# Performance work log

Hardware: AMD Instinct MI355X
Metric: run time of the kernel (lower is better)

The kernel has to match this reference:

```python
import jax, jax.numpy as jnp
import numpy as np

B, D, T = 8192, 1024, 3          # batch, input_dim, num_tasks
E, HM, OM = 8, 2048, 512         # mmoe: experts, hidden, output
P, S, HC, OC = 3, 4, 1024, 256   # ple: specific, shared, hidden, output
TH, OUT = 256, 1                 # tower hidden, out_dim per task
EPS = 1e-5


def _ln(h):
    mu = jnp.mean(h, axis=-1, keepdims=True)
    v = jnp.mean((h - mu) ** 2, axis=-1, keepdims=True)
    return (h - mu) * jax.lax.rsqrt(v + EPS)


def setup_inputs() -> dict:
    key = jax.random.key(0)
    ks = iter(jax.random.split(key, 64))
    def w(*shape):
        return 0.02 * jax.random.normal(next(ks), shape, jnp.float32)
    z = lambda *s: jnp.zeros(s, jnp.float32)
    o = lambda *s: jnp.ones(s, jnp.float32)
    return {
        "x": jax.random.normal(next(ks), (B, D), jnp.float32),
        "mmoe_w1": w(E, D, HM), "mmoe_b1": z(E, HM), "mmoe_g": o(E, HM), "mmoe_be": z(E, HM),
        "mmoe_w2": w(E, HM, OM), "mmoe_b2": z(E, OM),
        "mmoe_gw": w(T, D, E), "mmoe_gb": z(T, E),
        "c0_sw1": w(S, OM, HC), "c0_sb1": z(S, HC), "c0_sg": o(S, HC), "c0_sbe": z(S, HC),
        "c0_sw2": w(S, HC, OC), "c0_sb2": z(S, OC),
        "c0_tw1": w(T, P, OM, HC), "c0_tb1": z(T, P, HC), "c0_tg": o(T, P, HC), "c0_tbe": z(T, P, HC),
        "c0_tw2": w(T, P, HC, OC), "c0_tb2": z(T, P, OC),
        "c0_gw": w(T, OM, P + S), "c0_gb": z(T, P + S),
        "c0_sgw": w(OM, T * P + S), "c0_sgb": z(T * P + S),
        "c1_sw1": w(S, OC, HC), "c1_sb1": z(S, HC), "c1_sg": o(S, HC), "c1_sbe": z(S, HC),
        "c1_sw2": w(S, HC, OC), "c1_sb2": z(S, OC),
        "c1_tw1": w(T, P, OC, HC), "c1_tb1": z(T, P, HC), "c1_tg": o(T, P, HC), "c1_tbe": z(T, P, HC),
        "c1_tw2": w(T, P, HC, OC), "c1_tb2": z(T, P, OC),
        "c1_gw": w(T, OC, P + S), "c1_gb": z(T, P + S),
        "tow_w1": w(T, OC, TH), "tow_b1": z(T, TH), "tow_w2": w(T, TH, OUT), "tow_b2": z(T, OUT),
    }


def _cgc(shared_in, task_in, sw1, sb1, sg, sbe, sw2, sb2,
         tw1, tb1, tg, tbe, tw2, tb2, gw, gb, sgw=None, sgb=None):
    # shared experts: [S, B, O]
    hs = jnp.einsum('bd,sdh->sbh', shared_in, sw1) + sb1[:, None, :]
    hs = jax.nn.relu(_ln(hs) * sg[:, None, :] + sbe[:, None, :])
    so = jnp.einsum('sbh,sho->sbo', hs, sw2) + sb2[:, None, :]
    # task-specific experts: [T, P, B, O]
    ht = jnp.einsum('tbd,tpdh->tpbh', task_in, tw1) + tb1[:, :, None, :]
    ht = jax.nn.relu(_ln(ht) * tg[:, :, None, :] + tbe[:, :, None, :])
    to = jnp.einsum('tpbh,tpho->tpbo', ht, tw2) + tb2[:, :, None, :]
    Tn, Pn, Bn, On = to.shape
    Sn = so.shape[0]
    # per-task expert bank: task-specific first, then shared (matches torch.cat order)
    ex = jnp.concatenate([to, jnp.broadcast_to(so[None], (Tn, Sn, Bn, On))], axis=1)
    gate = jax.nn.softmax(jnp.einsum('tbd,tde->tbe', task_in, gw) + gb[:, None, :], axis=-1)
    task_out = jnp.einsum('tbe,tebo->tbo', gate, ex)
    if sgw is None:
        return None, task_out
    all_ex = jnp.concatenate([to.reshape(Tn * Pn, Bn, On), so], axis=0)
    sgate = jax.nn.softmax(shared_in @ sgw + sgb, axis=-1)
    shared_out = jnp.einsum('be,ebo->bo', sgate, all_ex)
    return shared_out, task_out


def _fwd(x, mmoe_w1, mmoe_b1, mmoe_g, mmoe_be, mmoe_w2, mmoe_b2, mmoe_gw, mmoe_gb,
         c0_sw1, c0_sb1, c0_sg, c0_sbe, c0_sw2, c0_sb2,
         c0_tw1, c0_tb1, c0_tg, c0_tbe, c0_tw2, c0_tb2, c0_gw, c0_gb, c0_sgw, c0_sgb,
         c1_sw1, c1_sb1, c1_sg, c1_sbe, c1_sw2, c1_sb2,
         c1_tw1, c1_tb1, c1_tg, c1_tbe, c1_tw2, c1_tb2, c1_gw, c1_gb,
         tow_w1, tow_b1, tow_w2, tow_b2):
    # --- MMoE layer (dropout = identity in eval) ---
    h = jnp.einsum('bd,edh->ebh', x, mmoe_w1) + mmoe_b1[:, None, :]
    h = jax.nn.relu(_ln(h) * mmoe_g[:, None, :] + mmoe_be[:, None, :])
    eo = jnp.einsum('ebh,eho->ebo', h, mmoe_w2) + mmoe_b2[:, None, :]  # [E,B,OM]
    gate = jax.nn.softmax(jnp.einsum('bd,tde->tbe', x, mmoe_gw) + mmoe_gb[:, None, :], axis=-1)
    task_hs = jnp.einsum('tbe,ebo->tbo', gate, eo)  # [T,B,OM]
    shared_h = jnp.mean(task_hs, axis=0)            # 'mean' aggregate
    # --- PLE CGC layers ---
    shared_h, task_hs = _cgc(shared_h, task_hs, c0_sw1, c0_sb1, c0_sg, c0_sbe, c0_sw2, c0_sb2,
                             c0_tw1, c0_tb1, c0_tg, c0_tbe, c0_tw2, c0_tb2, c0_gw, c0_gb, c0_sgw, c0_sgb)
    _, task_hs = _cgc(shared_h, task_hs, c1_sw1, c1_sb1, c1_sg, c1_sbe, c1_sw2, c1_sb2,
                      c1_tw1, c1_tb1, c1_tg, c1_tbe, c1_tw2, c1_tb2, c1_gw, c1_gb)
    # --- task towers ---
    th = jax.nn.relu(jnp.einsum('tbo,toh->tbh', task_hs, tow_w1) + tow_b1[:, None, :])
    return jnp.einsum('tbh,tho->tbo', th, tow_w2) + tow_b2[:, None, :]  # [T,B,OUT]


def reference(x, mmoe_w1, mmoe_b1, mmoe_g, mmoe_be, mmoe_w2, mmoe_b2, mmoe_gw, mmoe_gb,
              c0_sw1, c0_sb1, c0_sg, c0_sbe, c0_sw2, c0_sb2,
              c0_tw1, c0_tb1, c0_tg, c0_tbe, c0_tw2, c0_tb2, c0_gw, c0_gb, c0_sgw, c0_sgb,
              c1_sw1, c1_sb1, c1_sg, c1_sbe, c1_sw2, c1_sb2,
              c1_tw1, c1_tb1, c1_tg, c1_tbe, c1_tw2, c1_tb2, c1_gw, c1_gb,
              tow_w1, tow_b1, tow_w2, tow_b2):
    return _fwd(x, mmoe_w1, mmoe_b1, mmoe_g, mmoe_be, mmoe_w2, mmoe_b2, mmoe_gw, mmoe_gb,
                c0_sw1, c0_sb1, c0_sg, c0_sbe, c0_sw2, c0_sb2,
                c0_tw1, c0_tb1, c0_tg, c0_tbe, c0_tw2, c0_tb2, c0_gw, c0_gb, c0_sgw, c0_sgb,
                c1_sw1, c1_sb1, c1_sg, c1_sbe, c1_sw2, c1_sb2,
                c1_tw1, c1_tb1, c1_tg, c1_tbe, c1_tw2, c1_tb2, c1_gw, c1_gb,
                tow_w1, tow_b1, tow_w2, tow_b2)
```

## Files before the change

kernel.cpp:

```cpp
#include <hip/hip_runtime.h>

typedef unsigned short u16;
typedef unsigned int   u32;
typedef __bf16  bf16x8 __attribute__((ext_vector_type(8)));
typedef float   f32x4  __attribute__((ext_vector_type(4)));

#define B_ 8192
#define DI __device__ __forceinline__

DI u16 f2bf(float f) {
  u32 u = __float_as_uint(f);
  u = (u + 0x7fffu + ((u >> 16) & 1u)) >> 16;
  return (u16)u;
}
DI float bf2f(u16 h) { return __uint_as_float(((u32)h) << 16); }

DI void gll(const u16* g, u16* l) {
  __builtin_amdgcn_global_load_lds(
      (const __attribute__((address_space(1))) void*)g,
      (__attribute__((address_space(3))) void*)l, 16, 0, 0);
}

__global__ __launch_bounds__(256) void transpose_cast(
    const float* __restrict__ W, u16* __restrict__ Wt, int K, int N) {
  __shared__ float tile[64][65];
  int g = blockIdx.z;
  int k0 = blockIdx.x * 64, n0 = blockIdx.y * 64;
  const float* Wg = W + (size_t)g * K * N;
  u16* Og = Wt + (size_t)g * N * K;
  int tid = threadIdx.x;
  int rr = tid >> 4, cc = (tid & 15) * 4;
#pragma unroll
  for (int r = 0; r < 4; ++r) {
    int k = rr + r * 16;
    float4 v = *(const float4*)(Wg + (size_t)(k0 + k) * N + n0 + cc);
    tile[k][cc] = v.x; tile[k][cc + 1] = v.y; tile[k][cc + 2] = v.z; tile[k][cc + 3] = v.w;
  }
  __syncthreads();
  int nr = tid >> 3, kc = (tid & 7) * 8;
#pragma unroll
  for (int p = 0; p < 2; ++p) {
    int n = nr + p * 32;
    u16 tmp[8];
#pragma unroll
    for (int j = 0; j < 8; ++j) tmp[j] = f2bf(tile[kc + j][n]);
    *(uint4*)(Og + (size_t)(n0 + n) * K + k0 + kc) = *(uint4*)tmp;
  }
}

__global__ __launch_bounds__(256) void cast_bf16k(const float* __restrict__ X, u16* __restrict__ Y) {
  size_t i = ((size_t)blockIdx.x * 256 + threadIdx.x) * 4;
  float4 v = *(const float4*)(X + i);
  u16 t[4] = { f2bf(v.x), f2bf(v.y), f2bf(v.z), f2bf(v.w) };
  *(uint2*)(Y + i) = *(uint2*)t;
}

#define BM 128
#define BK 32
#define LDK 32

template<int BN_>
__global__ __launch_bounds__(256) void gemm_t(
    const u16* __restrict__ A, long a_stride, int a_div, int a_g0,
    const u16* __restrict__ Wt, const float* __restrict__ bias,
    u16* __restrict__ C, long c_stride, int N, int K, int relu_flag) {
  constexpr int JT = BN_ / 32;
  constexpr int BROWS = BN_ / 4;
  int gz = blockIdx.z;
  const u16* Ag = A + (size_t)((a_g0 + gz) / a_div) * a_stride;
  const u16* Wg = Wt + (size_t)gz * N * K;
  u16* Cg = C + (size_t)gz * c_stride;
  int m0 = blockIdx.x * BM, n0 = blockIdx.y * BN_;

  __shared__ __align__(16) u16 As[BM * LDK];
  __shared__ __align__(16) u16 Bs[BN_ * LDK];

  int tid = threadIdx.x;
  int wv = tid >> 6, ln = tid & 63;
  int wm = (wv >> 1) * 64, wn = (wv & 1) * (BN_ / 2);
  int lr = ln & 15, lk = (ln >> 4) * 8;

  int sr = ln >> 2;
  int sc = (ln & 3) * 8;
  const u16* aG = Ag + (size_t)(m0 + wv * 32 + sr) * K + sc;
  const u16* bG = Wg + (size_t)(n0 + wv * BROWS + sr) * K + sc;
  u16* aL0 = As + (wv * 32) * LDK;
  u16* aL1 = aL0 + 16 * LDK;
  u16* bL0 = Bs + (wv * BROWS) * LDK;

  f32x4 acc[4][JT];
#pragma unroll
  for (int i = 0; i < 4; ++i)
#pragma unroll
    for (int j = 0; j < JT; ++j)
      acc[i][j] = (f32x4){0.f, 0.f, 0.f, 0.f};

  int nk = K / BK;
  for (int ks = 0; ks < nk; ++ks) {
    __syncthreads();
    gll(aG + ks * BK, aL0);
    gll(aG + ks * BK + (size_t)16 * K, aL1);
    gll(bG + ks * BK, bL0);
    if (BN_ == 128) gll(bG + ks * BK + (size_t)16 * K, bL0 + 16 * LDK);
    __syncthreads();
    bf16x8 af[4], bfr[JT];
#pragma unroll
    for (int i = 0; i < 4; ++i) {
      union { uint4 u; bf16x8 v; } ua;
      ua.u = *(const uint4*)(As + (wm + i * 16 + lr) * LDK + lk);
      af[i] = ua.v;
    }
#pragma unroll
    for (int j = 0; j < JT; ++j) {
      union { uint4 u; bf16x8 v; } ub;
      ub.u = *(const uint4*)(Bs + (wn + j * 16 + lr) * LDK + lk);
      bfr[j] = ub.v;
    }
#pragma unroll
    for (int i = 0; i < 4; ++i)
#pragma unroll
      for (int j = 0; j < JT; ++j)
        acc[i][j] = __builtin_amdgcn_mfma_f32_16x16x32_bf16(af[i], bfr[j], acc[i][j], 0, 0, 0);
  }

  int mr = (ln >> 4) * 4;
#pragma unroll
  for (int i = 0; i < 4; ++i) {
#pragma unroll
    for (int j = 0; j < JT; ++j) {
      int n = n0 + wn + j * 16 + lr;
      float bv = bias[(size_t)gz * N + n];
#pragma unroll
      for (int r = 0; r < 4; ++r) {
        int m = m0 + wm + i * 16 + mr + r;
        float v = acc[i][j][r] + bv;
        if (relu_flag) v = fmaxf(v, 0.f);
        Cg[(size_t)m * N + n] = f2bf(v);
      }
    }
  }
}

__global__ __launch_bounds__(256) void ln_affine_relu(
    u16* __restrict__ H, const float* __restrict__ gain, const float* __restrict__ beta, int N) {
  __shared__ float red[4];
  size_t row = blockIdx.x;
  int grp = (int)(row / B_);
  u16* hp = H + row * N;
  const float* gp = gain + (size_t)grp * N;
  const float* bp = beta + (size_t)grp * N;
  int tid = threadIdx.x;
  int nw = blockDim.x >> 6;
  union { uint4 u; u16 s[8]; } pk;
  pk.u = *(const uint4*)(hp + tid * 8);
  float v[8], s = 0.f;
#pragma unroll
  for (int j = 0; j < 8; ++j) { v[j] = bf2f(pk.s[j]); s += v[j]; }
  for (int off = 32; off > 0; off >>= 1) s += __shfl_down(s, off, 64);
  if ((tid & 63) == 0) red[tid >> 6] = s;
  __syncthreads();
  float tot = 0.f;
  for (int i = 0; i < nw; ++i) tot += red[i];
  float mu = tot / (float)N;
  float q = 0.f;
#pragma unroll
  for (int j = 0; j < 8; ++j) { float d = v[j] - mu; q += d * d; }
  __syncthreads();
  for (int off = 32; off > 0; off >>= 1) q += __shfl_down(q, off, 64);
  if ((tid & 63) == 0) red[tid >> 6] = q;
  __syncthreads();
  tot = 0.f;
  for (int i = 0; i < nw; ++i) tot += red[i];
  float rstd = rsqrtf(tot / (float)N + 1e-5f);
  float4 ga = *(const float4*)(gp + tid * 8);
  float4 gb2 = *(const float4*)(gp + tid * 8 + 4);
  float4 ba = *(const float4*)(bp + tid * 8);
  float4 bb2 = *(const float4*)(bp + tid * 8 + 4);
  float gg[8] = { ga.x, ga.y, ga.z, ga.w, gb2.x, gb2.y, gb2.z, gb2.w };
  float bt[8] = { ba.x, ba.y, ba.z, ba.w, bb2.x, bb2.y, bb2.z, bb2.w };
  u16 o[8];
#pragma unroll
  for (int j = 0; j < 8; ++j) {
    float y = (v[j] - mu) * rstd * gg[j] + bt[j];
    o[j] = f2bf(fmaxf(y, 0.f));
  }
  *(uint4*)(hp + tid * 8) = *(uint4*)o;
}

__global__ __launch_bounds__(256) void prep_gw4(
    const float* __restrict__ W, float* __restrict__ out4,
    int G, int K, int E, int L) {
  int id = blockIdx.x * 256 + threadIdx.x;
  int tot = (K >> 2) * 32;
  if (id >= tot) return;
  int k4 = id >> 5, j = id & 31;
  int t = j / L, e = j % L;
  float4 v = { 0.f, 0.f, 0.f, 0.f };
  if (t < G && e < E) {
    const float* w = W + (size_t)t * K * E + e;
    v.x = w[(size_t)(k4 * 4 + 0) * E];
    v.y = w[(size_t)(k4 * 4 + 1) * E];
    v.z = w[(size_t)(k4 * 4 + 2) * E];
    v.w = w[(size_t)(k4 * 4 + 3) * E];
  }
  *(float4*)(out4 + (size_t)id * 4) = v;
}

__global__ __launch_bounds__(256) void gates_fast(
    const void* __restrict__ X, int is_bf16, long t_stride,
    const float* __restrict__ GW4, const float* __restrict__ GB,
    float* __restrict__ out, int G, int K, int E, int L) {
  int tid = threadIdx.x;
  int rl = tid >> 5;
  int j  = tid & 31;
  int t = j / L, e = j % L;
  int b = blockIdx.x * 8 + rl;
  int tr = (t < G) ? t : (G - 1);
  int K4 = K >> 2;
  float ac0 = 0.f, ac1 = 0.f, ac2 = 0.f, ac3 = 0.f;
  if (is_bf16) {
    const u16* xr = (const u16*)X + (size_t)tr * t_stride + (size_t)b * K;
    for (int k4 = 0; k4 < K4; k4 += 4) {
      uint2 p0 = *(const uint2*)(xr + (k4 + 0) * 4);
      uint2 p1 = *(const uint2*)(xr + (k4 + 1) * 4);
      uint2 p2 = *(const uint2*)(xr + (k4 + 2) * 4);
      uint2 p3 = *(const uint2*)(xr + (k4 + 3) * 4);
      float4 q0 = *(const float4*)(GW4 + ((size_t)(k4 + 0) * 32 + j) * 4);
      float4 q1 = *(const float4*)(GW4 + ((size_t)(k4 + 1) * 32 + j) * 4);
      float4 q2 = *(const float4*)(GW4 + ((size_t)(k4 + 2) * 32 + j) * 4);
      float4 q3 = *(const float4*)(GW4 + ((size_t)(k4 + 3) * 32 + j) * 4);
      ac0 += bf2f((u16)(p0.x & 0xffffu)) * q0.x + bf2f((u16)(p0.x >> 16)) * q0.y
           + bf2f((u16)(p0.y & 0xffffu)) * q0.z + bf2f((u16)(p0.y >> 16)) * q0.w;
      ac1 += bf2f((u16)(p1.x & 0xffffu)) * q1.x + bf2f((u16)(p1.x >> 16)) * q1.y
           + bf2f((u16)(p1.y & 0xffffu)) * q1.z + bf2f((u16)(p1.y >> 16)) * q1.w;
      ac2 += bf2f((u16)(p2.x & 0xffffu)) * q2.x + bf2f((u16)(p2.x >> 16)) * q2.y
           + bf2f((u16)(p2.y & 0xffffu)) * q2.z + bf2f((u16)(p2.y >> 16)) * q2.w;
      ac3 += bf2f((u16)(p3.x & 0xffffu)) * q3.x + bf2f((u16)(p3.x >> 16)) * q3.y
           + bf2f((u16)(p3.y & 0xffffu)) * q3.z + bf2f((u16)(p3.y >> 16)) * q3.w;
    }
  } else {
    const float* xr = (const float*)X + (size_t)tr * t_stride + (size_t)b * K;
    for (int k4 = 0; k4 < K4; k4 += 4) {
      float4 x0 = *(const float4*)(xr + (k4 + 0) * 4);
      float4 x1 = *(const float4*)(xr + (k4 + 1) * 4);
      float4 x2 = *(const float4*)(xr + (k4 + 2) * 4);
      float4 x3 = *(const float4*)(xr + (k4 + 3) * 4);
      float4 q0 = *(const float4*)(GW4 + ((size_t)(k4 + 0) * 32 + j) * 4);
      float4 q1 = *(const float4*)(GW4 + ((size_t)(k4 + 1) * 32 + j) * 4);
      float4 q2 = *(const float4*)(GW4 + ((size_t)(k4 + 2) * 32 + j) * 4);
      float4 q3 = *(const float4*)(GW4 + ((size_t)(k4 + 3) * 32 + j) * 4);
      ac0 += x0.x * q0.x + x0.y * q0.y + x0.z * q0.z + x0.w * q0.w;
      ac1 += x1.x * q1.x + x1.y * q1.y + x1.z * q1.z + x1.w * q1.w;
      ac2 += x2.x * q2.x + x2.y * q2.y + x2.z * q2.z + x2.w * q2.w;
      ac3 += x3.x * q3.x + x3.y * q3.y + x3.z * q3.z + x3.w * q3.w;
    }
  }
  float acc = (ac0 + ac1) + (ac2 + ac3);
  bool valid = (t < G) && (e < E);
  float lg = valid ? (acc + GB[t * E + e]) : -1e30f;
  float m = lg;
  for (int o = L >> 1; o > 0; o >>= 1) m = fmaxf(m, __shfl_xor(m, o, L));
  float ex = valid ? expf(lg - m) : 0.f;
  float sm = ex;
  for (int o = L >> 1; o > 0; o >>= 1) sm += __shfl_xor(sm, o, L);
  if (valid) out[((size_t)t * B_ + b) * E + e] = ex / sm;
}

__global__ __launch_bounds__(256) void mmoe_mix(
    const u16* __restrict__ eo, const float* __restrict__ gates,
    u16* __restrict__ task_hs, u16* __restrict__ shared_h) {
  __shared__ float g[24];
  int b = blockIdx.x, tid = threadIdx.x;
  if (tid < 24) g[tid] = gates[((size_t)(tid >> 3) * B_ + b) * 8 + (tid & 7)];
  __syncthreads();
  int o = tid * 2;
  float a0[3] = {0, 0, 0}, a1[3] = {0, 0, 0};
#pragma unroll
  for (int e = 0; e < 8; ++e) {
    u32 w = *(const u32*)(eo + ((size_t)e * B_ + b) * 512 + o);
    float v0 = bf2f((u16)(w & 0xffffu)), v1 = bf2f((u16)(w >> 16));
#pragma unroll
    for (int t = 0; t < 3; ++t) { a0[t] += g[t * 8 + e] * v0; a1[t] += g[t * 8 + e] * v1; }
  }
  float s0 = 0.f, s1 = 0.f;
#pragma unroll
  for (int t = 0; t < 3; ++t) {
    u16 p[2] = { f2bf(a0[t]), f2bf(a1[t]) };
    *(u32*)(task_hs + ((size_t)t * B_ + b) * 512 + o) = *(u32*)p;
    s0 += a0[t]; s1 += a1[t];
  }
  u16 p[2] = { f2bf(s0 * (1.f / 3.f)), f2bf(s1 * (1.f / 3.f)) };
  *(u32*)(shared_h + (size_t)b * 512 + o) = *(u32*)p;
}

__global__ __launch_bounds__(256) void cgc_mix(
    const u16* __restrict__ to, const u16* __restrict__ so,
    const float* __restrict__ g, const float* __restrict__ sg,
    u16* __restrict__ task_out, u16* __restrict__ shared_out) {
  int b = blockIdx.x, o = threadIdx.x;
  float tv[9], sv[4];
#pragma unroll
  for (int j = 0; j < 9; ++j) tv[j] = bf2f(to[((size_t)j * B_ + b) * 256 + o]);
#pragma unroll
  for (int s = 0; s < 4; ++s) sv[s] = bf2f(so[((size_t)s * B_ + b) * 256 + o]);
#pragma unroll
  for (int t = 0; t < 3; ++t) {
    const float* gt = g + ((size_t)t * B_ + b) * 7;
    float a = gt[0] * tv[t * 3] + gt[1] * tv[t * 3 + 1] + gt[2] * tv[t * 3 + 2];
#pragma unroll
    for (int s = 0; s < 4; ++s) a += gt[3 + s] * sv[s];
    task_out[((size_t)t * B_ + b) * 256 + o] = f2bf(a);
  }
  if (shared_out) {
    const float* sp = sg + (size_t)b * 13;
    float a = 0.f;
#pragma unroll
    for (int j = 0; j < 9; ++j) a += sp[j] * tv[j];
#pragma unroll
    for (int s = 0; s < 4; ++s) a += sp[9 + s] * sv[s];
    shared_out[(size_t)b * 256 + o] = f2bf(a);
  }
}

__global__ __launch_bounds__(256) void tower_out(
    const u16* __restrict__ th, const float* __restrict__ w2,
    const float* __restrict__ b2, float* __restrict__ out) {
  int r = blockIdx.x * 4 + (threadIdx.x >> 6);
  int lane = threadIdx.x & 63;
  int t = r / B_;
  const u16* row = th + (size_t)r * 256;
  u16 hv[4];
  *(uint2*)hv = *(const uint2*)(row + lane * 4);
  float4 wv = *(const float4*)(w2 + t * 256 + lane * 4);
  float s = bf2f(hv[0]) * wv.x + bf2f(hv[1]) * wv.y + bf2f(hv[2]) * wv.z + bf2f(hv[3]) * wv.w;
  for (int off = 32; off > 0; off >>= 1) s += __shfl_down(s, off, 64);
  if (lane == 0) out[r] = s + b2[t];
}

extern "C" void kernel_launch(void* const* d_in, const int* in_sizes, int n_in,
                              void* d_out, int out_size, void* d_ws, size_t ws_size,
                              hipStream_t stream) {
  (void)in_sizes; (void)n_in; (void)out_size;
  const float* x      = (const float*)d_in[0];
  const float* m_w1   = (const float*)d_in[1];
  const float* m_b1   = (const float*)d_in[2];
  const float* m_g    = (const float*)d_in[3];
  const float* m_be   = (const float*)d_in[4];
  const float* m_w2   = (const float*)d_in[5];
  const float* m_b2   = (const float*)d_in[6];
  const float* m_gw   = (const float*)d_in[7];
  const float* m_gb   = (const float*)d_in[8];
  const float* c0_sw1 = (const float*)d_in[9];
  const float* c0_sb1 = (const float*)d_in[10];
  const float* c0_sg  = (const float*)d_in[11];
  const float* c0_sbe = (const float*)d_in[12];
  const float* c0_sw2 = (const float*)d_in[13];
  const float* c0_sb2 = (const float*)d_in[14];
  const float* c0_tw1 = (const float*)d_in[15];
  const float* c0_tb1 = (const float*)d_in[16];
  const float* c0_tg  = (const float*)d_in[17];
  const float* c0_tbe = (const float*)d_in[18];
  const float* c0_tw2 = (const float*)d_in[19];
  const float* c0_tb2 = (const float*)d_in[20];
  const float* c0_gw  = (const float*)d_in[21];
  const float* c0_gb  = (const float*)d_in[22];
  const float* c0_sgw = (const float*)d_in[23];
  const float* c0_sgb = (const float*)d_in[24];
  const float* c1_sw1 = (const float*)d_in[25];
  const float* c1_sb1 = (const float*)d_in[26];
  const float* c1_sg  = (const float*)d_in[27];
  const float* c1_sbe = (const float*)d_in[28];
  const float* c1_sw2 = (const float*)d_in[29];
  const float* c1_sb2 = (const float*)d_in[30];
  const float* c1_tw1 = (const float*)d_in[31];
  const float* c1_tb1 = (const float*)d_in[32];
  const float* c1_tg  = (const float*)d_in[33];
  const float* c1_tbe = (const float*)d_in[34];
  const float* c1_tw2 = (const float*)d_in[35];
  const float* c1_tb2 = (const float*)d_in[36];
  const float* c1_gw  = (const float*)d_in[37];
  const float* c1_gb  = (const float*)d_in[38];
  const float* tw1    = (const float*)d_in[39];
  const float* tb1    = (const float*)d_in[40];
  const float* tw2    = (const float*)d_in[41];
  const float* tb2    = (const float*)d_in[42];

  const size_t MB = 1024 * 1024;
  char* ws = (char*)d_ws;
  size_t off = 0;
  u16* arena = (u16*)(ws + off); off += 24 * MB;
  u16* eoR   = (u16*)(ws + off); off += 64 * MB;
  u16* hbuf  = (u16*)(ws + off); off += 32 * MB;
  u16* thsR  = (u16*)(ws + off); off += 24 * MB;
  u16* xbR   = (u16*)(ws + off); off += 16 * MB;
  u16* shR   = (u16*)(ws + off); off += 8 * MB;
  float* gmo = (float*)(ws + off); off += 3 * MB;
  if (ws_size < off) return;

  float* g0  = gmo + (size_t)3 * B_ * 8;
  float* sg0 = g0  + (size_t)3 * B_ * 7;
  float* g1  = sg0 + (size_t)B_ * 13;

  u16* xb       = xbR;
  u16* eo       = eoR;
  u16* task_hs  = thsR;
  u16* shared_h = shR;
  u16* soD      = eoR;
  u16* toD      = eoR + (size_t)4 * B_ * 256;
  u16* task1    = xbR;
  u16* shared1  = xbR + (size_t)3 * B_ * 256;
  u16* task2    = thsR;
  u16* thbuf    = hbuf;

  float* gw4a = (float*)hbuf;
  float* gw4b = (float*)hbuf + 32768;

  dim3 blk(256);
  cast_bf16k<<<8192, blk, 0, stream>>>(x, xb);

  prep_gw4<<<32, blk, 0, stream>>>(m_gw, gw4a, 3, 1024, 8, 8);
  gates_fast<<<B_ / 8, blk, 0, stream>>>(x, 0, 0L, gw4a, m_gb, gmo, 3, 1024, 8, 8);

  {
    u16* w1t_lo = arena;
    u16* w2t_lo = arena + (size_t)4 * 2048 * 1024;
    u16* w1t_hi = thsR;
    u16* w2t_hi = thsR + (size_t)4 * 2048 * 1024;
    transpose_cast<<<dim3(16, 32, 4), blk, 0, stream>>>(m_w1, w1t_lo, 1024, 2048);
    transpose_cast<<<dim3(32,  8, 4), blk, 0, stream>>>(m_w2, w2t_lo, 2048, 512);
    transpose_cast<<<dim3(16, 32, 4), blk, 0, stream>>>(m_w1 + (size_t)4 * 1024 * 2048, w1t_hi, 1024, 2048);
    transpose_cast<<<dim3(32,  8, 4), blk, 0, stream>>>(m_w2 + (size_t)4 * 2048 * 512,  w2t_hi, 2048, 512);
    for (int e = 0; e < 8; ++e) {
      u16* w1t = (e < 4 ? w1t_lo : w1t_hi) + (size_t)(e & 3) * 2048 * 1024;
      u16* w2t = (e < 4 ? w2t_lo : w2t_hi) + (size_t)(e & 3) * 512 * 2048;
      gemm_t<128><<<dim3(64, 16, 1), blk, 0, stream>>>(
          xb, 0L, 1, 0, w1t, m_b1 + (size_t)e * 2048, hbuf, 0L, 2048, 1024, 0);
      ln_affine_relu<<<B_, 256, 0, stream>>>(hbuf, m_g + (size_t)e * 2048, m_be + (size_t)e * 2048, 2048);
      gemm_t<64><<<dim3(64, 8, 1), blk, 0, stream>>>(
          hbuf, 0L, 1, 0, w2t, m_b2 + (size_t)e * 512,
          eo + (size_t)e * B_ * 512, 0L, 512, 2048, 0);
    }
  }
  mmoe_mix<<<B_, blk, 0, stream>>>(eo, gmo, task_hs, shared_h);

  prep_gw4<<<16, blk, 0, stream>>>(c0_gw, gw4a, 3, 512, 7, 8);
  prep_gw4<<<16, blk, 0, stream>>>(c0_sgw, gw4b, 1, 512, 13, 16);
  gates_fast<<<B_ / 8, blk, 0, stream>>>(task_hs, 1, (long)B_ * 512, gw4a, c0_gb, g0, 3, 512, 7, 8);
  gates_fast<<<B_ / 8, blk, 0, stream>>>(shared_h, 1, 0L, gw4b, c0_sgb, sg0, 1, 512, 13, 16);

  {
    u16* sw1t = arena;
    u16* sw2t = sw1t + (size_t)4 * 1024 * 512;
    u16* tw1t = sw2t + (size_t)4 * 256 * 1024;
    u16* tw2t = tw1t + (size_t)9 * 1024 * 512;
    transpose_cast<<<dim3( 8, 16, 4), blk, 0, stream>>>(c0_sw1, sw1t, 512, 1024);
    transpose_cast<<<dim3(16,  4, 4), blk, 0, stream>>>(c0_sw2, sw2t, 1024, 256);
    transpose_cast<<<dim3( 8, 16, 9), blk, 0, stream>>>(c0_tw1, tw1t, 512, 1024);
    transpose_cast<<<dim3(16,  4, 9), blk, 0, stream>>>(c0_tw2, tw2t, 1024, 256);
    for (int g0i = 0; g0i < 4; g0i += 2) {
      gemm_t<128><<<dim3(64, 8, 2), blk, 0, stream>>>(
          shared_h, 0L, 1, 0, sw1t + (size_t)g0i * 1024 * 512, c0_sb1 + (size_t)g0i * 1024,
          hbuf, (long)B_ * 1024, 1024, 512, 0);
      ln_affine_relu<<<2 * B_, 128, 0, stream>>>(hbuf, c0_sg + (size_t)g0i * 1024, c0_sbe + (size_t)g0i * 1024, 1024);
      gemm_t<64><<<dim3(64, 4, 2), blk, 0, stream>>>(
          hbuf, (long)B_ * 1024, 1, 0, sw2t + (size_t)g0i * 256 * 1024, c0_sb2 + (size_t)g0i * 256,
          soD + (size_t)g0i * B_ * 256, (long)B_ * 256, 256, 1024, 0);
    }
    for (int g0i = 0; g0i < 9; g0i += 2) {
      int gsz = (g0i + 2 <= 9) ? 2 : 1;
      gemm_t<128><<<dim3(64, 8, gsz), blk, 0, stream>>>(
          task_hs, (long)B_ * 512, 3, g0i, tw1t + (size_t)g0i * 1024 * 512, c0_tb1 + (size_t)g0i * 1024,
          hbuf, (long)B_ * 1024, 1024, 512, 0);
      ln_affine_relu<<<gsz * B_, 128, 0, stream>>>(hbuf, c0_tg + (size_t)g0i * 1024, c0_tbe + (size_t)g0i * 1024, 1024);
      gemm_t<64><<<dim3(64, 4, gsz), blk, 0, stream>>>(
          hbuf, (long)B_ * 1024, 1, 0, tw2t + (size_t)g0i * 256 * 1024, c0_tb2 + (size_t)g0i * 256,
          toD + (size_t)g0i * B_ * 256, (long)B_ * 256, 256, 1024, 0);
    }
  }
  cgc_mix<<<B_, blk, 0, stream>>>(toD, soD, g0, sg0, task1, shared1);

  prep_gw4<<<8, blk, 0, stream>>>(c1_gw, gw4a, 3, 256, 7, 8);
  gates_fast<<<B_ / 8, blk, 0, stream>>>(task1, 1, (long)B_ * 256, gw4a, c1_gb, g1, 3, 256, 7, 8);

  {
    u16* sw1t = arena;
    u16* sw2t = sw1t + (size_t)4 * 1024 * 256;
    u16* tw1t = sw2t + (size_t)4 * 256 * 1024;
    u16* tw2t = tw1t + (size_t)9 * 1024 * 256;
    transpose_cast<<<dim3( 4, 16, 4), blk, 0, stream>>>(c1_sw1, sw1t, 256, 1024);
    transpose_cast<<<dim3(16,  4, 4), blk, 0, stream>>>(c1_sw2, sw2t, 1024, 256);
    transpose_cast<<<dim3( 4, 16, 9), blk, 0, stream>>>(c1_tw1, tw1t, 256, 1024);
    transpose_cast<<<dim3(16,  4, 9), blk, 0, stream>>>(c1_tw2, tw2t, 1024, 256);
    for (int g0i = 0; g0i < 4; g0i += 2) {
      gemm_t<128><<<dim3(64, 8, 2), blk, 0, stream>>>(
          shared1, 0L, 1, 0, sw1t + (size_t)g0i * 1024 * 256, c1_sb1 + (size_t)g0i * 1024,
          hbuf, (long)B_ * 1024, 1024, 256, 0);
      ln_affine_relu<<<2 * B_, 128, 0, stream>>>(hbuf, c1_sg + (size_t)g0i * 1024, c1_sbe + (size_t)g0i * 1024, 1024);
      gemm_t<64><<<dim3(64, 4, 2), blk, 0, stream>>>(
          hbuf, (long)B_ * 1024, 1, 0, sw2t + (size_t)g0i * 256 * 1024, c1_sb2 + (size_t)g0i * 256,
          soD + (size_t)g0i * B_ * 256, (long)B_ * 256, 256, 1024, 0);
    }
    for (int g0i = 0; g0i < 9; g0i += 2) {
      int gsz = (g0i + 2 <= 9) ? 2 : 1;
      gemm_t<128><<<dim3(64, 8, gsz), blk, 0, stream>>>(
          task1, (long)B_ * 256, 3, g0i, tw1t + (size_t)g0i * 1024 * 256, c1_tb1 + (size_t)g0i * 1024,
          hbuf, (long)B_ * 1024, 1024, 256, 0);
      ln_affine_relu<<<gsz * B_, 128, 0, stream>>>(hbuf, c1_tg + (size_t)g0i * 1024, c1_tbe + (size_t)g0i * 1024, 1024);
      gemm_t<64><<<dim3(64, 4, gsz), blk, 0, stream>>>(
          hbuf, (long)B_ * 1024, 1, 0, tw2t + (size_t)g0i * 256 * 1024, c1_tb2 + (size_t)g0i * 256,
          toD + (size_t)g0i * B_ * 256, (long)B_ * 256, 256, 1024, 0);
    }
  }
  cgc_mix<<<B_, blk, 0, stream>>>(toD, soD, g1, nullptr, task2, nullptr);

  {
    u16* twt = arena;
    transpose_cast<<<dim3(4, 4, 3), blk, 0, stream>>>(tw1, twt, 256, 256);
    gemm_t<64><<<dim3(64, 4, 3), blk, 0, stream>>>(
        task2, (long)B_ * 256, 1, 0, twt, tb1, thbuf, (long)B_ * 256, 256, 256, 1);
    tower_out<<<6144, blk, 0, stream>>>(thbuf, tw2, tb2, (float*)d_out);
  }
}
```

Measured before the change: 2.227 ms.

## Batch experts into single launches with row-chunked schedule and new workspace layout

```diff
diff --git a/kernel.cpp b/kernel.cpp
--- a/kernel.cpp
+++ b/kernel.cpp
@@ -142,10 +142,11 @@
 }
 
 __global__ __launch_bounds__(256) void ln_affine_relu(
-    u16* __restrict__ H, const float* __restrict__ gain, const float* __restrict__ beta, int N) {
+    u16* __restrict__ H, const float* __restrict__ gain, const float* __restrict__ beta,
+    int N, int rows_per_group) {
   __shared__ float red[4];
   size_t row = blockIdx.x;
-  int grp = (int)(row / B_);
+  int grp = (int)(row / (size_t)rows_per_group);
   u16* hp = H + row * N;
   const float* gp = gain + (size_t)grp * N;
   const float* bp = beta + (size_t)grp * N;
@@ -217,45 +218,38 @@
   int b = blockIdx.x * 8 + rl;
   int tr = (t < G) ? t : (G - 1);
   int K4 = K >> 2;
-  float ac0 = 0.f, ac1 = 0.f, ac2 = 0.f, ac3 = 0.f;
+  float ac[8];
+#pragma unroll
+  for (int u = 0; u < 8; ++u) ac[u] = 0.f;
   if (is_bf16) {
     const u16* xr = (const u16*)X + (size_t)tr * t_stride + (size_t)b * K;
-    for (int k4 = 0; k4 < K4; k4 += 4) {
-      uint2 p0 = *(const uint2*)(xr + (k4 + 0) * 4);
-      uint2 p1 = *(const uint2*)(xr + (k4 + 1) * 4);
-      uint2 p2 = *(const uint2*)(xr + (k4 + 2) * 4);
-      uint2 p3 = *(const uint2*)(xr + (k4 + 3) * 4);
-      float4 q0 = *(const float4*)(GW4 + ((size_t)(k4 + 0) * 32 + j) * 4);
-      float4 q1 = *(const float4*)(GW4 + ((size_t)(k4 + 1) * 32 + j) * 4);
-      float4 q2 = *(const float4*)(GW4 + ((size_t)(k4 + 2) * 32 + j) * 4);
-      float4 q3 = *(const float4*)(GW4 + ((size_t)(k4 + 3) * 32 + j) * 4);
-      ac0 += bf2f((u16)(p0.x & 0xffffu)) * q0.x + bf2f((u16)(p0.x >> 16)) * q0.y
-           + bf2f((u16)(p0.y & 0xffffu)) * q0.z + bf2f((u16)(p0.y >> 16)) * q0.w;
-      ac1 += bf2f((u16)(p1.x & 0xffffu)) * q1.x + bf2f((u16)(p1.x >> 16)) * q1.y
-           + bf2f((u16)(p1.y & 0xffffu)) * q1.z + bf2f((u16)(p1.y >> 16)) * q1.w;
-      ac2 += bf2f((u16)(p2.x & 0xffffu)) * q2.x + bf2f((u16)(p2.x >> 16)) * q2.y
-           + bf2f((u16)(p2.y & 0xffffu)) * q2.z + bf2f((u16)(p2.y >> 16)) * q2.w;
-      ac3 += bf2f((u16)(p3.x & 0xffffu)) * q3.x + bf2f((u16)(p3.x >> 16)) * q3.y
-           + bf2f((u16)(p3.y & 0xffffu)) * q3.z + bf2f((u16)(p3.y >> 16)) * q3.w;
+    for (int k4 = 0; k4 < K4; k4 += 8) {
+      uint2 p[8]; float4 q[8];
+#pragma unroll
+      for (int u = 0; u < 8; ++u) {
+        p[u] = *(const uint2*)(xr + (k4 + u) * 4);
+        q[u] = *(const float4*)(GW4 + ((size_t)(k4 + u) * 32 + j) * 4);
+      }
+#pragma unroll
+      for (int u = 0; u < 8; ++u)
+        ac[u] += bf2f((u16)(p[u].x & 0xffffu)) * q[u].x + bf2f((u16)(p[u].x >> 16)) * q[u].y
+               + bf2f((u16)(p[u].y & 0xffffu)) * q[u].z + bf2f((u16)(p[u].y >> 16)) * q[u].w;
     }
   } else {
     const float* xr = (const float*)X + (size_t)tr * t_stride + (size_t)b * K;
-    for (int k4 = 0; k4 < K4; k4 += 4) {
-      float4 x0 = *(const float4*)(xr + (k4 + 0) * 4);
-      float4 x1 = *(const float4*)(xr + (k4 + 1) * 4);
-      float4 x2 = *(const float4*)(xr + (k4 + 2) * 4);
-      float4 x3 = *(const float4*)(xr + (k4 + 3) * 4);
-      float4 q0 = *(const float4*)(GW4 + ((size_t)(k4 + 0) * 32 + j) * 4);
-      float4 q1 = *(const float4*)(GW4 + ((size_t)(k4 + 1) * 32 + j) * 4);
-      float4 q2 = *(const float4*)(GW4 + ((size_t)(k4 + 2) * 32 + j) * 4);
-      float4 q3 = *(const float4*)(GW4 + ((size_t)(k4 + 3) * 32 + j) * 4);
-      ac0 += x0.x * q0.x + x0.y * q0.y + x0.z * q0.z + x0.w * q0.w;
-      ac1 += x1.x * q1.x + x1.y * q1.y + x1.z * q1.z + x1.w * q1.w;
-      ac2 += x2.x * q2.x + x2.y * q2.y + x2.z * q2.z + x2.w * q2.w;
-      ac3 += x3.x * q3.x + x3.y * q3.y + x3.z * q3.z + x3.w * q3.w;
+    for (int k4 = 0; k4 < K4; k4 += 8) {
+      float4 xv[8]; float4 q[8];
+#pragma unroll
+      for (int u = 0; u < 8; ++u) {
+        xv[u] = *(const float4*)(xr + (k4 + u) * 4);
+        q[u] = *(const float4*)(GW4 + ((size_t)(k4 + u) * 32 + j) * 4);
+      }
+#pragma unroll
+      for (int u = 0; u < 8; ++u)
+        ac[u] += xv[u].x * q[u].x + xv[u].y * q[u].y + xv[u].z * q[u].z + xv[u].w * q[u].w;
     }
   }
-  float acc = (ac0 + ac1) + (ac2 + ac3);
+  float acc = ((ac[0] + ac[1]) + (ac[2] + ac[3])) + ((ac[4] + ac[5]) + (ac[6] + ac[7]));
   bool valid = (t < G) && (e < E);
   float lg = valid ? (acc + GB[t * E + e]) : -1e30f;
   float m = lg;
@@ -387,137 +381,114 @@
 
   const size_t MB = 1024 * 1024;
   char* ws = (char*)d_ws;
-  size_t off = 0;
-  u16* arena = (u16*)(ws + off); off += 24 * MB;
-  u16* eoR   = (u16*)(ws + off); off += 64 * MB;
-  u16* hbuf  = (u16*)(ws + off); off += 32 * MB;
-  u16* thsR  = (u16*)(ws + off); off += 24 * MB;
-  u16* xbR   = (u16*)(ws + off); off += 16 * MB;
-  u16* shR   = (u16*)(ws + off); off += 8 * MB;
-  float* gmo = (float*)(ws + off); off += 3 * MB;
-  if (ws_size < off) return;
-
-  float* g0  = gmo + (size_t)3 * B_ * 8;
-  float* sg0 = g0  + (size_t)3 * B_ * 7;
-  float* g1  = sg0 + (size_t)B_ * 13;
-
-  u16* xb       = xbR;
-  u16* eo       = eoR;
-  u16* task_hs  = thsR;
-  u16* shared_h = shR;
-  u16* soD      = eoR;
-  u16* toD      = eoR + (size_t)4 * B_ * 256;
-  u16* task1    = xbR;
-  u16* shared1  = xbR + (size_t)3 * B_ * 256;
-  u16* task2    = thsR;
-  u16* thbuf    = hbuf;
-
-  float* gw4a = (float*)hbuf;
-  float* gw4b = (float*)hbuf + 32768;
+  if (ws_size < 163 * MB) return;
+  u16* XB      = (u16*)(ws);
+  u16* W1T     = (u16*)(ws + 16 * MB);
+  u16* W2T     = (u16*)(ws + 48 * MB);
+  u16* HID     = (u16*)(ws + 64 * MB);
+  u16* EO      = (u16*)(ws + 96 * MB);
+  u16* TASK_HS = (u16*)(ws + 16 * MB);
+  u16* SHARED_H= (u16*)(ws + 40 * MB);
+  u16* SO0     = (u16*)(ws);
+  u16* C0_SW1T = (u16*)(ws + 48 * MB);
+  u16* C0_SW2T = (u16*)(ws + 52 * MB);
+  u16* C0_TW1T = (u16*)(ws + 54 * MB);
+  u16* C0_TW2T = (u16*)(ws + 63 * MB);
+  u16* HID0    = (u16*)(ws + 68 * MB);
+  u16* TO0     = (u16*)(ws + 104 * MB);
+  u16* TASK1   = (u16*)(ws + 16 * MB);
+  u16* SHARED1 = (u16*)(ws + 28 * MB);
+  u16* SO1     = (u16*)(ws);
+  u16* C1_SW1T = (u16*)(ws + 48 * MB);
+  u16* C1_SW2T = (u16*)(ws + 50 * MB);
+  u16* C1_TW1T = (u16*)(ws + 52 * MB);
+  u16* C1_TW2T = (u16*)(ws + 56 * MB + 512 * 1024);
+  u16* HID1    = (u16*)(ws + 68 * MB);
+  u16* TO1     = (u16*)(ws + 104 * MB);
+  u16* TASK2   = (u16*)(ws + 32 * MB);
+  u16* TWT     = (u16*)(ws + 48 * MB);
+  u16* TH      = (u16*)(ws + 104 * MB);
+
+  float* gbase = (float*)(ws + 160 * MB);
+  float* gmo  = gbase;
+  float* g0   = gmo  + (size_t)3 * B_ * 8;
+  float* sg0  = g0   + (size_t)3 * B_ * 7;
+  float* g1   = sg0  + (size_t)B_ * 13;
+  float* gw4a = g1   + (size_t)3 * B_ * 7;
+  float* gw4b = gw4a + 32768;
 
   dim3 blk(256);
-  cast_bf16k<<<8192, blk, 0, stream>>>(x, xb);
+  cast_bf16k<<<8192, blk, 0, stream>>>(x, XB);
 
   prep_gw4<<<32, blk, 0, stream>>>(m_gw, gw4a, 3, 1024, 8, 8);
   gates_fast<<<B_ / 8, blk, 0, stream>>>(x, 0, 0L, gw4a, m_gb, gmo, 3, 1024, 8, 8);
 
-  {
-    u16* w1t_lo = arena;
-    u16* w2t_lo = arena + (size_t)4 * 2048 * 1024;
-    u16* w1t_hi = thsR;
-    u16* w2t_hi = thsR + (size_t)4 * 2048 * 1024;
-    transpose_cast<<<dim3(16, 32, 4), blk, 0, stream>>>(m_w1, w1t_lo, 1024, 2048);
-    transpose_cast<<<dim3(32,  8, 4), blk, 0, stream>>>(m_w2, w2t_lo, 2048, 512);
-    transpose_cast<<<dim3(16, 32, 4), blk, 0, stream>>>(m_w1 + (size_t)4 * 1024 * 2048, w1t_hi, 1024, 2048);
-    transpose_cast<<<dim3(32,  8, 4), blk, 0, stream>>>(m_w2 + (size_t)4 * 2048 * 512,  w2t_hi, 2048, 512);
-    for (int e = 0; e < 8; ++e) {
-      u16* w1t = (e < 4 ? w1t_lo : w1t_hi) + (size_t)(e & 3) * 2048 * 1024;
-      u16* w2t = (e < 4 ? w2t_lo : w2t_hi) + (size_t)(e & 3) * 512 * 2048;
-      gemm_t<128><<<dim3(64, 16, 1), blk, 0, stream>>>(
-          xb, 0L, 1, 0, w1t, m_b1 + (size_t)e * 2048, hbuf, 0L, 2048, 1024, 0);
-      ln_affine_relu<<<B_, 256, 0, stream>>>(hbuf, m_g + (size_t)e * 2048, m_be + (size_t)e * 2048, 2048);
-      gemm_t<64><<<dim3(64, 8, 1), blk, 0, stream>>>(
-          hbuf, 0L, 1, 0, w2t, m_b2 + (size_t)e * 512,
-          eo + (size_t)e * B_ * 512, 0L, 512, 2048, 0);
-    }
-  }
-  mmoe_mix<<<B_, blk, 0, stream>>>(eo, gmo, task_hs, shared_h);
+  transpose_cast<<<dim3(16, 32, 8), blk, 0, stream>>>(m_w1, W1T, 1024, 2048);
+  transpose_cast<<<dim3(32,  8, 8), blk, 0, stream>>>(m_w2, W2T, 2048, 512);
+  for (int c = 0; c < 8; ++c) {
+    size_t r0 = (size_t)c * 1024;
+    gemm_t<128><<<dim3(8, 16, 8), blk, 0, stream>>>(
+        XB + r0 * 1024, 0L, 1, 0, W1T, m_b1, HID, (long)1024 * 2048, 2048, 1024, 0);
+    ln_affine_relu<<<8 * 1024, 256, 0, stream>>>(HID, m_g, m_be, 2048, 1024);
+    gemm_t<64><<<dim3(8, 8, 8), blk, 0, stream>>>(
+        HID, (long)1024 * 2048, 1, 0, W2T, m_b2, EO + r0 * 512, (long)B_ * 512, 512, 2048, 0);
+  }
+  mmoe_mix<<<B_, blk, 0, stream>>>(EO, gmo, TASK_HS, SHARED_H);
 
   prep_gw4<<<16, blk, 0, stream>>>(c0_gw, gw4a, 3, 512, 7, 8);
   prep_gw4<<<16, blk, 0, stream>>>(c0_sgw, gw4b, 1, 512, 13, 16);
-  gates_fast<<<B_ / 8, blk, 0, stream>>>(task_hs, 1, (long)B_ * 512, gw4a, c0_gb, g0, 3, 512, 7, 8);
-  gates_fast<<<B_ / 8, blk, 0, stream>>>(shared_h, 1, 0L, gw4b, c0_sgb, sg0, 1, 512, 13, 16);
-
-  {
-    u16* sw1t = arena;
-    u16* sw2t = sw1t + (size_t)4 * 1024 * 512;
-    u16* tw1t = sw2t + (size_t)4 * 256 * 1024;
-    u16* tw2t = tw1t + (size_t)9 * 1024 * 512;
-    transpose_cast<<<dim3( 8, 16, 4), blk, 0, stream>>>(c0_sw1, sw1t, 512, 1024);
-    transpose_cast<<<dim3(16,  4, 4), blk, 0, stream>>>(c0_sw2, sw2t, 1024, 256);
-    transpose_cast<<<dim3( 8, 16, 9), blk, 0, stream>>>(c0_tw1, tw1t, 512, 1024);
-    transpose_cast<<<dim3(16,  4, 9), blk, 0, stream>>>(c0_tw2, tw2t, 1024, 256);
-    for (int g0i = 0; g0i < 4; g0i += 2) {
-      gemm_t<128><<<dim3(64, 8, 2), blk, 0, stream>>>(
-          shared_h, 0L, 1, 0, sw1t + (size_t)g0i * 1024 * 512, c0_sb1 + (size_t)g0i * 1024,
-          hbuf, (long)B_ * 1024, 1024, 512, 0);
-      ln_affine_relu<<<2 * B_, 128, 0, stream>>>(hbuf, c0_sg + (size_t)g0i * 1024, c0_sbe + (size_t)g0i * 1024, 1024);
-      gemm_t<64><<<dim3(64, 4, 2), blk, 0, stream>>>(
-          hbuf, (long)B_ * 1024, 1, 0, sw2t + (size_t)g0i * 256 * 1024, c0_sb2 + (size_t)g0i * 256,
-          soD + (size_t)g0i * B_ * 256, (long)B_ * 256, 256, 1024, 0);
-    }
-    for (int g0i = 0; g0i < 9; g0i += 2) {
-      int gsz = (g0i + 2 <= 9) ? 2 : 1;
-      gemm_t<128><<<dim3(64, 8, gsz), blk, 0, stream>>>(
-          task_hs, (long)B_ * 512, 3, g0i, tw1t + (size_t)g0i * 1024 * 512, c0_tb1 + (size_t)g0i * 1024,
-          hbuf, (long)B_ * 1024, 1024, 512, 0);
-      ln_affine_relu<<<gsz * B_, 128, 0, stream>>>(hbuf, c0_tg + (size_t)g0i * 1024, c0_tbe + (size_t)g0i * 1024, 1024);
-      gemm_t<64><<<dim3(64, 4, gsz), blk, 0, stream>>>(
-          hbuf, (long)B_ * 1024, 1, 0, tw2t + (size_t)g0i * 256 * 1024, c0_tb2 + (size_t)g0i * 256,
-          toD + (size_t)g0i * B_ * 256, (long)B_ * 256, 256, 1024, 0);
-    }
-  }
-  cgc_mix<<<B_, blk, 0, stream>>>(toD, soD, g0, sg0, task1, shared1);
+  gates_fast<<<B_ / 8, blk, 0, stream>>>(TASK_HS, 1, (long)B_ * 512, gw4a, c0_gb, g0, 3, 512, 7, 8);
+  gates_fast<<<B_ / 8, blk, 0, stream>>>(SHARED_H, 1, 0L, gw4b, c0_sgb, sg0, 1, 512, 13, 16);
+
+  transpose_cast<<<dim3( 8, 16, 4), blk, 0, stream>>>(c0_sw1, C0_SW1T, 512, 1024);
+  transpose_cast<<<dim3(16,  4, 4), blk, 0, stream>>>(c0_sw2, C0_SW2T, 1024, 256);
+  transpose_cast<<<dim3( 8, 16, 9), blk, 0, stream>>>(c0_tw1, C0_TW1T, 512, 1024);
+  transpose_cast<<<dim3(16,  4, 9), blk, 0, stream>>>(c0_tw2, C0_TW2T, 1024, 256);
+  for (int c = 0; c < 2; ++c) {
+    size_t r0 = (size_t)c * 4096;
+    gemm_t<128><<<dim3(32, 8, 4), blk, 0, stream>>>(
+        SHARED_H + r0 * 512, 0L, 1, 0, C0_SW1T, c0_sb1, HID0, (long)4096 * 1024, 1024, 512, 0);
+    ln_affine_relu<<<4 * 4096, 128, 0, stream>>>(HID0, c0_sg, c0_sbe, 1024, 4096);
+    gemm_t<64><<<dim3(32, 4, 4), blk, 0, stream>>>(
+        HID0, (long)4096 * 1024, 1, 0, C0_SW2T, c0_sb2, SO0 + r0 * 256, (long)B_ * 256, 256, 1024, 0);
+  }
+  for (int c = 0; c < 4; ++c) {
+    size_t r0 = (size_t)c * 2048;
+    gemm_t<128><<<dim3(16, 8, 9), blk, 0, stream>>>(
+        TASK_HS + r0 * 512, (long)B_ * 512, 3, 0, C0_TW1T, c0_tb1, HID0, (long)2048 * 1024, 1024, 512, 0);
+    ln_affine_relu<<<9 * 2048, 128, 0, stream>>>(HID0, c0_tg, c0_tbe, 1024, 2048);
+    gemm_t<64><<<dim3(16, 4, 9), blk, 0, stream>>>(
+        HID0, (long)2048 * 1024, 1, 0, C0_TW2T, c0_tb2, TO0 + r0 * 256, (long)B_ * 256, 256, 1024, 0);
+  }
+  cgc_mix<<<B_, blk, 0, stream>>>(TO0, SO0, g0, sg0, TASK1, SHARED1);
 
   prep_gw4<<<8, blk, 0, stream>>>(c1_gw, gw4a, 3, 256, 7, 8);
-  gates_fast<<<B_ / 8, blk, 0, stream>>>(task1, 1, (long)B_ * 256, gw4a, c1_gb, g1, 3, 256, 7, 8);
-
-  {
-    u16* sw1t = arena;
-    u16* sw2t = sw1t + (size_t)4 * 1024 * 256;
-    u16* tw1t = sw2t + (size_t)4 * 256 * 1024;
-    u16* tw2t = tw1t + (size_t)9 * 1024 * 256;
-    transpose_cast<<<dim3( 4, 16, 4), blk, 0, stream>>>(c1_sw1, sw1t, 256, 1024);
-    transpose_cast<<<dim3(16,  4, 4), blk, 0, stream>>>(c1_sw2, sw2t, 1024, 256);
-    transpose_cast<<<dim3( 4, 16, 9), blk, 0, stream>>>(c1_tw1, tw1t, 256, 1024);
-    transpose_cast<<<dim3(16,  4, 9), blk, 0, stream>>>(c1_tw2, tw2t, 1024, 256);
-    for (int g0i = 0; g0i < 4; g0i += 2) {
-      gemm_t<128><<<dim3(64, 8, 2), blk, 0, stream>>>(
-          shared1, 0L, 1, 0, sw1t + (size_t)g0i * 1024 * 256, c1_sb1 + (size_t)g0i * 1024,
-          hbuf, (long)B_ * 1024, 1024, 256, 0);
-      ln_affine_relu<<<2 * B_, 128, 0, stream>>>(hbuf, c1_sg + (size_t)g0i * 1024, c1_sbe + (size_t)g0i * 1024, 1024);
-      gemm_t<64><<<dim3(64, 4, 2), blk, 0, stream>>>(
-          hbuf, (long)B_ * 1024, 1, 0, sw2t + (size_t)g0i * 256 * 1024, c1_sb2 + (size_t)g0i * 256,
-          soD + (size_t)g0i * B_ * 256, (long)B_ * 256, 256, 1024, 0);
-    }
-    for (int g0i = 0; g0i < 9; g0i += 2) {
-      int gsz = (g0i + 2 <= 9) ? 2 : 1;
-      gemm_t<128><<<dim3(64, 8, gsz), blk, 0, stream>>>(
-          task1, (long)B_ * 256, 3, g0i, tw1t + (size_t)g0i * 1024 * 256, c1_tb1 + (size_t)g0i * 1024,
-          hbuf, (long)B_ * 1024, 1024, 256, 0);
-      ln_affine_relu<<<gsz * B_, 128, 0, stream>>>(hbuf, c1_tg + (size_t)g0i * 1024, c1_tbe + (size_t)g0i * 1024, 1024);
-      gemm_t<64><<<dim3(64, 4, gsz), blk, 0, stream>>>(
-          hbuf, (long)B_ * 1024, 1, 0, tw2t + (size_t)g0i * 256 * 1024, c1_tb2 + (size_t)g0i * 256,
-          toD + (size_t)g0i * B_ * 256, (long)B_ * 256, 256, 1024, 0);
-    }
-  }
-  cgc_mix<<<B_, blk, 0, stream>>>(toD, soD, g1, nullptr, task2, nullptr);
-
-  {
-    u16* twt = arena;
-    transpose_cast<<<dim3(4, 4, 3), blk, 0, stream>>>(tw1, twt, 256, 256);
-    gemm_t<64><<<dim3(64, 4, 3), blk, 0, stream>>>(
-        task2, (long)B_ * 256, 1, 0, twt, tb1, thbuf, (long)B_ * 256, 256, 256, 1);
-    tower_out<<<6144, blk, 0, stream>>>(thbuf, tw2, tb2, (float*)d_out);
-  }
-}
+  gates_fast<<<B_ / 8, blk, 0, stream>>>(TASK1, 1, (long)B_ * 256, gw4a, c1_gb, g1, 3, 256, 7, 8);
+
+  transpose_cast<<<dim3( 4, 16, 4), blk, 0, stream>>>(c1_sw1, C1_SW1T, 256, 1024);
+  transpose_cast<<<dim3(16,  4, 4), blk, 0, stream>>>(c1_sw2, C1_SW2T, 1024, 256);
+  transpose_cast<<<dim3( 4, 16, 9), blk, 0, stream>>>(c1_tw1, C1_TW1T, 256, 1024);
+  transpose_cast<<<dim3(16,  4, 9), blk, 0, stream>>>(c1_tw2, C1_TW2T, 1024, 256);
+  for (int c = 0; c < 2; ++c) {
+    size_t r0 = (size_t)c * 4096;
+    gemm_t<128><<<dim3(32, 8, 4), blk, 0, stream>>>(
+        SHARED1 + r0 * 256, 0L, 1, 0, C1_SW1T, c1_sb1, HID1, (long)4096 * 1024, 1024, 256, 0);
+    ln_affine_relu<<<4 * 4096, 128, 0, stream>>>(HID1, c1_sg, c1_sbe, 1024, 4096);
+    gemm_t<64><<<dim3(32, 4, 4), blk, 0, stream>>>(
+        HID1, (long)4096 * 1024, 1, 0, C1_SW2T, c1_sb2, SO1 + r0 * 256, (long)B_ * 256, 256, 1024, 0);
+  }
+  for (int c = 0; c < 4; ++c) {
+    size_t r0 = (size_t)c * 2048;
+    gemm_t<128><<<dim3(16, 8, 9), blk, 0, stream>>>(
+        TASK1 + r0 * 256, (long)B_ * 256, 3, 0, C1_TW1T, c1_tb1, HID1, (long)2048 * 1024, 1024, 256, 0);
+    ln_affine_relu<<<9 * 2048, 128, 0, stream>>>(HID1, c1_tg, c1_tbe, 1024, 2048);
+    gemm_t<64><<<dim3(16, 4, 9), blk, 0, stream>>>(
+        HID1, (long)2048 * 1024, 1, 0, C1_TW2T, c1_tb2, TO1 + r0 * 256, (long)B_ * 256, 256, 1024, 0);
+  }
+  cgc_mix<<<B_, blk, 0, stream>>>(TO1, SO1, g1, nullptr, TASK2, nullptr);
+
+  transpose_cast<<<dim3(4, 4, 3), blk, 0, stream>>>(tw1, TWT, 256, 256);
+  gemm_t<64><<<dim3(64, 4, 3), blk, 0, stream>>>(
+      TASK2, (long)B_ * 256, 1, 0, TWT, tb1, TH, (long)B_ * 256, 256, 256, 1);
+  tower_out<<<6144, blk, 0, stream>>>(TH, tw2, tb2, (float*)d_out);
+}
```

New measurement: 2.247 ms. About the same (+0.9%).
